# Performance work log

Measured on AMD Instinct MI355X. Metric: run time of the kernel, lower is better.

The kernel has to match this reference:

```python
import jax, jax.numpy as jnp
import numpy as np

B, C, H = 65536, 512, 8
HD = C // H  # head dim = 64
SCALE = HD ** -0.5


def setup_inputs() -> dict:
    key = jax.random.key(0)
    k1, k2, k3, k4 = jax.random.split(key, 4)
    x = jax.random.normal(k1, (B, 2, C), dtype=jnp.float32)
    W_kv = jax.random.normal(k2, (C, 2 * C), dtype=jnp.float32) * (C ** -0.5)
    W_proj = jax.random.normal(k3, (C, C), dtype=jnp.float32) * (C ** -0.5)
    b_proj = jax.random.normal(k4, (C,), dtype=jnp.float32) * 0.01
    return {"x": x, "W_kv": W_kv, "W_proj": W_proj, "b_proj": b_proj}


def _kv(tok, W_kv):
    # tok: [B, N, C] -> k, v each [B, H, N, hd]
    b, n, c = tok.shape
    kv = (tok @ W_kv).reshape(b, n, 2, H, HD)          # [B,N,2,H,hd]
    kv = jnp.transpose(kv, (2, 0, 3, 1, 4))            # [2,B,H,N,hd]
    return kv[0], kv[1]


def reference(x, W_kv, W_proj, b_proj):
    x_img = x[:, :1, :]   # [B,1,C]
    x_pps = x[:, 1:, :]   # [B,N,C], N==1 (required by original reshape)
    b, n, c = x_pps.shape

    k_img, v_img = _kv(x_img, W_kv)   # [B,H,N,hd] each
    k_pps, v_pps = _kv(x_pps, W_kv)

    q = jnp.transpose(x_pps.reshape(b, n, H, HD), (0, 2, 1, 3))  # [B,H,N,hd]

    attn = jnp.einsum('bhqd,bhkd->bhqk', q, k_pps) * SCALE
    attn = jax.nn.softmax(attn, axis=-1)
    out = jnp.einsum('bhqk,bhkd->bhqd', attn, v_img)             # [B,H,N,hd]
    out = jnp.transpose(out, (0, 2, 1, 3)).reshape(b, n, c)       # [B,N,C]
    return out @ W_proj + b_proj
```

## Files before the change

kernel.cpp:

```cpp
#include <hip/hip_runtime.h>
#include <stdint.h>

typedef __attribute__((ext_vector_type(4))) float f32x4;
typedef __attribute__((ext_vector_type(8))) __bf16 bf16x8;
typedef __attribute__((ext_vector_type(4))) unsigned short u16x4;

static __device__ __forceinline__ unsigned short f2bf(float f) {
  union { float f; uint32_t u; } v; v.f = f;
  return (unsigned short)((v.u + 0x7fffu + ((v.u >> 16) & 1u)) >> 16);
}

__global__ __launch_bounds__(256) void prep_wc(
    const float* __restrict__ W_kv, const float* __restrict__ W_proj,
    unsigned short* __restrict__ WcPack)
{
  const int t = threadIdx.x;
  const int k0 = blockIdx.x * 4;
  const int col = t & 127;
  const int n = col * 4;
  const int kj = __builtin_amdgcn_readfirstlane((t >> 7) * 2);
  const float* __restrict__ wv0 = W_kv + (size_t)(k0 + kj) * 1024 + 512;
  const float* __restrict__ wv1 = W_kv + (size_t)(k0 + kj + 1) * 1024 + 512;

  float acc0[4] = {0.f, 0.f, 0.f, 0.f};
  float acc1[4] = {0.f, 0.f, 0.f, 0.f};
  #pragma unroll 4
  for (int c = 0; c < 512; ++c) {
    const float a0 = wv0[c];
    const float a1 = wv1[c];
    const f32x4 p = *reinterpret_cast<const f32x4*>(W_proj + (size_t)c * 512 + n);
    #pragma unroll
    for (int i = 0; i < 4; ++i) { acc0[i] += a0 * p[i]; acc1[i] += a1 * p[i]; }
  }

  #pragma unroll
  for (int j = 0; j < 2; ++j) {
    const int k = k0 + kj + j;
    const int ks = k >> 6, kk = k & 63;
    const float* a = j ? acc1 : acc0;
    #pragma unroll
    for (int i = 0; i < 4; ++i) {
      const int nn = n + i;
      const int ct = nn >> 7, cc = nn & 127;
      const uint32_t boff = (uint32_t)(((cc << 7) + (kk << 1)) ^ ((cc & 7) << 4));
      WcPack[(size_t)(((ct << 3) + ks) << 13) + (boff >> 1)] = f2bf(a[i]);
    }
  }
}

__global__ __launch_bounds__(256, 2) void gemm_main(
    const float* __restrict__ x, const unsigned short* __restrict__ WcPack,
    const float* __restrict__ b_proj, float* __restrict__ out)
{
  __shared__ unsigned short Alds[2][128 * 64];
  __shared__ unsigned short Blds[2][128 * 64];

  const int tid = threadIdx.x;
  const int bid = blockIdx.x;
  const int m0 = (bid >> 2) << 7;
  const int ct = bid & 3;
  const int n0 = ct << 7;

  const int lane = tid & 63;
  const int wave = tid >> 6;
  const int wr = wave >> 1, wc = wave & 1;
  const int l15 = lane & 15, l4 = lane >> 4;

  f32x4 acc[4][4] = {};

  const int arow = tid >> 4;
  const int af4 = tid & 15;

  auto issueB = [&](int bufi, int kt) {
    const char* g = reinterpret_cast<const char*>(WcPack) + (((ct << 3) + kt) << 14);
    char* l = reinterpret_cast<char*>(&Blds[bufi][0]);
    #pragma unroll
    for (int i = 0; i < 4; ++i) {
      const int off = (i << 12) + (tid << 4);
      __builtin_amdgcn_global_load_lds(
          (__attribute__((address_space(1))) void*)(void*)(g + off),
          (__attribute__((address_space(3))) void*)(void*)(l + off),
          16, 0, 0);
    }
  };
  auto loadA = [&](int kt, f32x4* tmp) {
    const float* src = x + (size_t)m0 * 1024 + (kt << 6);
    #pragma unroll
    for (int p = 0; p < 8; ++p) {
      const int row = arow + (p << 4);
      tmp[p] = *reinterpret_cast<const f32x4*>(src + (size_t)row * 1024 + (af4 << 2));
    }
  };
  auto writeA = [&](int bufi, const f32x4* tmp) {
    char* base = reinterpret_cast<char*>(&Alds[bufi][0]);
    #pragma unroll
    for (int p = 0; p < 8; ++p) {
      const int row = arow + (p << 4);
      const uint32_t boff = (uint32_t)(((row << 7) + (af4 << 3)) ^ ((row & 7) << 4));
      u16x4 h;
      h.x = f2bf(tmp[p][0]); h.y = f2bf(tmp[p][1]);
      h.z = f2bf(tmp[p][2]); h.w = f2bf(tmp[p][3]);
      *reinterpret_cast<u16x4*>(base + boff) = h;
    }
  };
  auto compute = [&](int bufi) {
    const char* Ab = reinterpret_cast<const char*>(&Alds[bufi][0]);
    const char* Bb = reinterpret_cast<const char*>(&Blds[bufi][0]);
    #pragma unroll
    for (int ks = 0; ks < 2; ++ks) {
      bf16x8 afr[4], bfr[4];
      #pragma unroll
      for (int i = 0; i < 4; ++i) {
        const int ar = (wr << 6) + (i << 4) + l15;
        const uint32_t ao = (uint32_t)(((ar << 7) + (ks << 6) + (l4 << 4)) ^ ((ar & 7) << 4));
        afr[i] = *reinterpret_cast<const bf16x8*>(Ab + ao);
        const int bc = (wc << 6) + (i << 4) + l15;
        const uint32_t bo = (uint32_t)(((bc << 7) + (ks << 6) + (l4 << 4)) ^ ((bc & 7) << 4));
        bfr[i] = *reinterpret_cast<const bf16x8*>(Bb + bo);
      }
      #pragma unroll
      for (int mi = 0; mi < 4; ++mi)
        #pragma unroll
        for (int ni = 0; ni < 4; ++ni)
          acc[mi][ni] = __builtin_amdgcn_mfma_f32_16x16x32_bf16(
              afr[mi], bfr[ni], acc[mi][ni], 0, 0, 0);
    }
  };

  {
    f32x4 tmp[8];
    issueB(0, 0);
    loadA(0, tmp);
    writeA(0, tmp);
  }
  __syncthreads();

  int buf = 0;
  for (int kt = 0; kt < 8; ++kt) {
    f32x4 nxt[8];
    if (kt < 7) { issueB(buf ^ 1, kt + 1); loadA(kt + 1, nxt); }
    compute(buf);
    if (kt < 7) writeA(buf ^ 1, nxt);
    __syncthreads();
    buf ^= 1;
  }

  const int cbase = n0 + (wc << 6) + l15;
  float bias[4];
  #pragma unroll
  for (int ni = 0; ni < 4; ++ni) bias[ni] = b_proj[cbase + (ni << 4)];
  const int rbase = m0 + (wr << 6) + (l4 << 2);
  #pragma unroll
  for (int mi = 0; mi < 4; ++mi) {
    #pragma unroll
    for (int ni = 0; ni < 4; ++ni) {
      const int cg = cbase + (ni << 4);
      #pragma unroll
      for (int rg = 0; rg < 4; ++rg) {
        const int row = rbase + (mi << 4) + rg;
        out[(size_t)row * 512 + cg] = acc[mi][ni][rg] + bias[ni];
      }
    }
  }
}

extern "C" void kernel_launch(void* const* d_in, const int* in_sizes, int n_in,
                              void* d_out, int out_size, void* d_ws, size_t ws_size,
                              hipStream_t stream) {
  const float* x      = (const float*)d_in[0];
  const float* W_kv   = (const float*)d_in[1];
  const float* W_proj = (const float*)d_in[2];
  const float* b_proj = (const float*)d_in[3];
  float* out = (float*)d_out;
  unsigned short* WcPack = (unsigned short*)d_ws;

  prep_wc<<<128, 256, 0, stream>>>(W_kv, W_proj, WcPack);
  gemm_main<<<2048, 256, 0, stream>>>(x, WcPack, b_proj, out);
}
```

Measured before the change: 496.2 us.

## Remap block order for XCD locality, split prep reduction, use native bf16 convert

Three separate changes. The main GEMM blockIdx is remapped so that consecutive hardware blocks, which are dispatched round-robin across XCDs, land on the same M-tile group, improving L2 reuse of the x rows shared by the four column tiles. The weight-fold prep kernel splits its 512-long reduction into two independent accumulator chains to expose more ILP. The A-tile float-to-bf16 conversion uses the compiler's native __bf16 cast, which may map to hardware convert instructions instead of manual integer rounding.

```diff
diff --git a/kernel.cpp b/kernel.cpp
--- a/kernel.cpp
+++ b/kernel.cpp
@@ -3,7 +3,7 @@
 
 typedef __attribute__((ext_vector_type(4))) float f32x4;
 typedef __attribute__((ext_vector_type(8))) __bf16 bf16x8;
-typedef __attribute__((ext_vector_type(4))) unsigned short u16x4;
+typedef __attribute__((ext_vector_type(4))) __bf16 bf16x4;
 
 static __device__ __forceinline__ unsigned short f2bf(float f) {
   union { float f; uint32_t u; } v; v.f = f;
@@ -20,30 +20,33 @@
   const int n = col * 4;
   const int kj = __builtin_amdgcn_readfirstlane((t >> 7) * 2);
   const float* __restrict__ wv0 = W_kv + (size_t)(k0 + kj) * 1024 + 512;
-  const float* __restrict__ wv1 = W_kv + (size_t)(k0 + kj + 1) * 1024 + 512;
+  const float* __restrict__ wv1 = wv0 + 1024;
 
-  float acc0[4] = {0.f, 0.f, 0.f, 0.f};
-  float acc1[4] = {0.f, 0.f, 0.f, 0.f};
+  float a0a[4] = {}, a0b[4] = {}, a1a[4] = {}, a1b[4] = {};
   #pragma unroll 4
-  for (int c = 0; c < 512; ++c) {
-    const float a0 = wv0[c];
-    const float a1 = wv1[c];
+  for (int c = 0; c < 256; ++c) {
+    const float s0 = wv0[c],        s1 = wv1[c];
+    const float t0 = wv0[c + 256],  t1 = wv1[c + 256];
     const f32x4 p = *reinterpret_cast<const f32x4*>(W_proj + (size_t)c * 512 + n);
+    const f32x4 q = *reinterpret_cast<const f32x4*>(W_proj + (size_t)(c + 256) * 512 + n);
     #pragma unroll
-    for (int i = 0; i < 4; ++i) { acc0[i] += a0 * p[i]; acc1[i] += a1 * p[i]; }
+    for (int i = 0; i < 4; ++i) {
+      a0a[i] += s0 * p[i]; a1a[i] += s1 * p[i];
+      a0b[i] += t0 * q[i]; a1b[i] += t1 * q[i];
+    }
   }
 
   #pragma unroll
   for (int j = 0; j < 2; ++j) {
     const int k = k0 + kj + j;
     const int ks = k >> 6, kk = k & 63;
-    const float* a = j ? acc1 : acc0;
     #pragma unroll
     for (int i = 0; i < 4; ++i) {
+      const float val = j ? (a1a[i] + a1b[i]) : (a0a[i] + a0b[i]);
       const int nn = n + i;
       const int ct = nn >> 7, cc = nn & 127;
       const uint32_t boff = (uint32_t)(((cc << 7) + (kk << 1)) ^ ((cc & 7) << 4));
-      WcPack[(size_t)(((ct << 3) + ks) << 13) + (boff >> 1)] = f2bf(a[i]);
+      WcPack[(size_t)(((ct << 3) + ks) << 13) + (boff >> 1)] = f2bf(val);
     }
   }
 }
@@ -56,7 +59,8 @@
   __shared__ unsigned short Blds[2][128 * 64];
 
   const int tid = threadIdx.x;
-  const int bid = blockIdx.x;
+  const int rawb = (int)blockIdx.x;
+  const int bid = ((rawb & 7) << 8) + (rawb >> 3);
   const int m0 = (bid >> 2) << 7;
   const int ct = bid & 3;
   const int n0 = ct << 7;
@@ -97,10 +101,10 @@
     for (int p = 0; p < 8; ++p) {
       const int row = arow + (p << 4);
       const uint32_t boff = (uint32_t)(((row << 7) + (af4 << 3)) ^ ((row & 7) << 4));
-      u16x4 h;
-      h.x = f2bf(tmp[p][0]); h.y = f2bf(tmp[p][1]);
-      h.z = f2bf(tmp[p][2]); h.w = f2bf(tmp[p][3]);
-      *reinterpret_cast<u16x4*>(base + boff) = h;
+      bf16x4 h;
+      h[0] = (__bf16)tmp[p][0]; h[1] = (__bf16)tmp[p][1];
+      h[2] = (__bf16)tmp[p][2]; h[3] = (__bf16)tmp[p][3];
+      *reinterpret_cast<bf16x4*>(base + boff) = h;
     }
   };
   auto compute = [&](int bufi) {
```

New measurement: 455.0 us. 8.3% less time.
